# Kernel tuning notes

Measured on AMD Instinct MI355X. Metric: run time of the kernel, lower is better.

The kernel has to match this reference:

```python
import jax, jax.numpy as jnp
import numpy as np

N = 100000   # nodes
E = 3200000  # edges
F = 128      # input features
H1 = 128     # first_gcn_dimensions
H2 = 64      # second_gcn_dimensions
D1 = 64      # first_dense_neurons
D2 = 8       # second_dense_neurons
L = 10       # number_of_labels


def setup_inputs() -> dict:
    key = jax.random.key(0)
    ks = jax.random.split(key, 8)
    edges = jax.random.randint(ks[0], (2, E), 0, N)
    features = jax.random.normal(ks[1], (N, F), dtype=jnp.float32)
    s = lambda k, shape: jax.random.normal(k, shape, dtype=jnp.float32) * 0.05
    return dict(
        edges=edges, features=features,
        W1=s(ks[2], (F, H1)), b1=jnp.zeros((H1,), jnp.float32),
        W2=s(ks[3], (H1, H2)), b2=jnp.zeros((H2,), jnp.float32),
        Wf1=s(ks[4], (H2, D1)), bf1=jnp.zeros((D1,), jnp.float32),
        Wf2=s(ks[5], (D1, D2)), bf2=jnp.zeros((D2,), jnp.float32),
        Wl=s(ks[6], (H2 * D2, L)), bl=jnp.zeros((L,), jnp.float32),
    )


def gcn_conv(x, W, b, src, dst, n):
    # PyG GCNConv: x' = D^{-1/2} (A + I) D^{-1/2} (x W) + b  (self-loops already in src/dst)
    h = x @ W                                            # [N, out]
    deg = jax.ops.segment_sum(jnp.ones(dst.shape[0], x.dtype), dst, num_segments=n)
    dinv = jnp.where(deg > 0, jax.lax.rsqrt(deg), 0.0)   # deg^{-1/2}, 0 for isolated
    norm = dinv[src] * dinv[dst]                         # [E+N]
    agg = jax.ops.segment_sum(h[src] * norm[:, None], dst, num_segments=n)
    return agg + b


def reference(edges, features, W1, b1, W2, b2, Wf1, bf1, Wf2, bf2, Wl, bl):
    n = features.shape[0]
    loop = jnp.arange(n)
    src = jnp.concatenate([edges[0], loop])
    dst = jnp.concatenate([edges[1], loop])

    h1 = jax.nn.relu(gcn_conv(features, W1, b1, src, dst, n))  # [N, H1]
    h2 = gcn_conv(h1, W2, b2, src, dst, n)                     # [N, H2]

    a1 = jnp.tanh(h2 @ Wf1 + bf1)                              # [N, D1]
    att = jax.nn.softmax(a1 @ Wf2 + bf2, axis=0)               # softmax over nodes, [N, D2]

    graph_embedding = (att.T @ h2).reshape(1, -1)              # [1, D2*H2]
    P = att.T @ att - jnp.eye(att.shape[1], dtype=att.dtype)   # [D2, D2]
    penalty = jnp.sum(jnp.sqrt(jnp.sum(P * P, axis=1)))

    predictions = jax.nn.log_softmax(graph_embedding @ Wl + bl, axis=1)  # [1, L]
    return graph_embedding, penalty, predictions
```

## Files before the change

### kernel.cpp

```cpp
#include <hip/hip_runtime.h>
#include <hip/hip_bf16.h>
#include <math.h>

#define NNODES 100000
#define NEDGES 3200000
#define NBUK ((NNODES + 127) >> 7)
#define NCHUNK 256
#define EPC (NEDGES / NCHUNK)

typedef float floatx2 __attribute__((ext_vector_type(2)));
typedef float f32x4 __attribute__((ext_vector_type(4)));
typedef short bf16x8 __attribute__((ext_vector_type(8)));

__device__ __forceinline__ unsigned short f2bf(float x) {
    unsigned u = __float_as_uint(x);
    unsigned r = u + 0x7FFFu + ((u >> 16) & 1u);
    return (unsigned short)(r >> 16);
}

__device__ __forceinline__ void acc8_fp8(uint2 v, floatx2* a) {
    a[0] += __builtin_amdgcn_cvt_pk_f32_fp8(v.x, false);
    a[1] += __builtin_amdgcn_cvt_pk_f32_fp8(v.x, true);
    a[2] += __builtin_amdgcn_cvt_pk_f32_fp8(v.y, false);
    a[3] += __builtin_amdgcn_cvt_pk_f32_fp8(v.y, true);
}
__device__ __forceinline__ void acc4_fp8(unsigned v, floatx2* a) {
    a[0] += __builtin_amdgcn_cvt_pk_f32_fp8(v, false);
    a[1] += __builtin_amdgcn_cvt_pk_f32_fp8(v, true);
}

__global__ void prep_w_kernel(const float* __restrict__ W1, const float* __restrict__ W2,
                              unsigned short* __restrict__ Wt1, unsigned short* __restrict__ Wt2) {
    int i = blockIdx.x * 256 + threadIdx.x;
    if (i < 128 * 128) {
        int k = i >> 7, n = i & 127;
        Wt1[n * 128 + k] = f2bf(W1[i]);
    } else if (i < 128 * 128 + 128 * 64) {
        int j = i - 128 * 128;
        int k = j >> 6, n = j & 63;
        Wt2[n * 128 + k] = f2bf(W2[j]);
    }
}

__global__ __launch_bounds__(1024) void chunk_hist_kernel(const int* __restrict__ dst,
                                                          int* __restrict__ hist) {
    __shared__ int h[NBUK];
    int c = blockIdx.x, t = threadIdx.x;
    for (int i = t; i < NBUK; i += 1024) h[i] = 0;
    __syncthreads();
    const int4* d4 = (const int4*)(dst + c * EPC);
    for (int i = t; i < EPC / 4; i += 1024) {
        int4 d = d4[i];
        atomicAdd(&h[d.x >> 7], 1);
        atomicAdd(&h[d.y >> 7], 1);
        atomicAdd(&h[d.z >> 7], 1);
        atomicAdd(&h[d.w >> 7], 1);
    }
    __syncthreads();
    for (int i = t; i < NBUK; i += 1024)
        hist[c * NBUK + i] = h[i];
}

__global__ void col_scan_kernel(int* __restrict__ hist, int* __restrict__ btot) {
    int t = blockIdx.x * 256 + threadIdx.x;
    if (t >= NBUK) return;
    int run = 0;
    for (int c = 0; c < NCHUNK; c++) {
        int idx = c * NBUK + t;
        int v = hist[idx];
        hist[idx] = run;
        run += v;
    }
    btot[t] = run;
}

__global__ void bucket_scan_kernel(const int* __restrict__ btot, int* __restrict__ bstart,
                                   int* __restrict__ row_start, float* __restrict__ smalls) {
    __shared__ int s[1024];
    int t = threadIdx.x;
    if (t < 592) smalls[t] = 0.0f;
    int v = (t < NBUK) ? btot[t] : 0;
    s[t] = v;
    __syncthreads();
    for (int off = 1; off < 1024; off <<= 1) {
        int x = (t >= off) ? s[t - off] : 0;
        __syncthreads();
        s[t] += x;
        __syncthreads();
    }
    if (t < NBUK) bstart[t] = s[t] - v;
    if (t == 0) {
        bstart[NBUK] = NEDGES;
        row_start[NNODES] = NEDGES;
    }
}

__global__ __launch_bounds__(1024) void chunk_scatter_kernel(const int* __restrict__ src,
                                                             const int* __restrict__ dst,
                                                             const int* __restrict__ hist,
                                                             const int* __restrict__ bstart,
                                                             int* __restrict__ ebuk) {
    __shared__ int cur[NBUK];
    int c = blockIdx.x, t = threadIdx.x;
    for (int i = t; i < NBUK; i += 1024)
        cur[i] = bstart[i] + hist[c * NBUK + i];
    __syncthreads();
    const int4* s4 = (const int4*)(src + c * EPC);
    const int4* d4 = (const int4*)(dst + c * EPC);
    for (int i = t; i < EPC / 4; i += 1024) {
        int4 s = s4[i];
        int4 d = d4[i];
        int p0 = atomicAdd(&cur[d.x >> 7], 1);
        ebuk[p0] = s.x | ((d.x & 127) << 20);
        int p1 = atomicAdd(&cur[d.y >> 7], 1);
        ebuk[p1] = s.y | ((d.y & 127) << 20);
        int p2 = atomicAdd(&cur[d.z >> 7], 1);
        ebuk[p2] = s.z | ((d.z & 127) << 20);
        int p3 = atomicAdd(&cur[d.w >> 7], 1);
        ebuk[p3] = s.w | ((d.w & 127) << 20);
    }
}

__global__ __launch_bounds__(256) void build_kernel(const int* __restrict__ ebuk,
                                                    const int* __restrict__ bstart,
                                                    int* __restrict__ row_start,
                                                    float* __restrict__ dinv,
                                                    int* __restrict__ csr) {
    __shared__ int cnt[128];
    __shared__ int scn[128];
    __shared__ int cur[128];
    int b = blockIdx.x;
    int t = threadIdx.x;
    int s0 = bstart[b], s1 = bstart[b + 1];
    if (t < 128) cnt[t] = 0;
    __syncthreads();
    for (int i = s0 + t; i < s1; i += 256)
        atomicAdd(&cnt[(ebuk[i] >> 20) & 127], 1);
    __syncthreads();
    if (t < 128) scn[t] = cnt[t];
    __syncthreads();
#pragma unroll
    for (int off = 1; off < 128; off <<= 1) {
        int x = (t < 128 && t >= off) ? scn[t - off] : 0;
        __syncthreads();
        if (t < 128) scn[t] += x;
        __syncthreads();
    }
    int node = b * 128 + t;
    if (t < 128) {
        int rs = s0 + scn[t] - cnt[t];
        cur[t] = rs;
        if (node < NNODES) {
            row_start[node] = rs;
            dinv[node] = rsqrtf((float)cnt[t] + 1.0f);
        }
    }
    __syncthreads();
    for (int i = s0 + t; i < s1; i += 256) {
        int v = ebuk[i];
        int pos = atomicAdd(&cur[(v >> 20) & 127], 1);
        csr[pos] = v & 0xFFFFF;
    }
}

template <int KIN, int KOUT, bool ABF16>
__global__ __launch_bounds__(256) void gemm_mfma_kernel(const void* __restrict__ Av,
                                                        const unsigned short* __restrict__ Wt,
                                                        const float* __restrict__ rowscale,
                                                        unsigned char* __restrict__ stage) {
    constexpr int LDK = KIN + 8;
    constexpr int LDC = KOUT + 4;
    constexpr int SH_AB = (64 + KOUT) * LDK * 2;
    constexpr int SH_C  = 64 * LDC * 4;
    constexpr int SH = SH_AB > SH_C ? SH_AB : SH_C;
    __shared__ char shbuf[SH];
    unsigned short* As = (unsigned short*)shbuf;
    unsigned short* Ws = As + 64 * LDK;
    float* Cs = (float*)shbuf;
    int t = threadIdx.x;
    int block_row = blockIdx.x * 64;

    for (int idx = t; idx < KOUT * (KIN / 8); idx += 256) {
        int n = idx / (KIN / 8), c = idx % (KIN / 8);
        *(uint4*)(Ws + n * LDK + c * 8) = *(const uint4*)(Wt + n * KIN + c * 8);
    }
    if (ABF16) {
        const unsigned short* A = (const unsigned short*)Av;
        for (int idx = t; idx < 64 * (KIN / 8); idx += 256) {
            int r = idx / (KIN / 8), c = idx % (KIN / 8);
            uint4 v = make_uint4(0, 0, 0, 0);
            if (block_row + r < NNODES)
                v = *(const uint4*)(A + (size_t)(block_row + r) * KIN + c * 8);
            *(uint4*)(As + r * LDK + c * 8) = v;
        }
    } else {
        const float* A = (const float*)Av;
        for (int idx = t; idx < 64 * (KIN / 4); idx += 256) {
            int r = idx / (KIN / 4), c = idx % (KIN / 4);
            float4 v = make_float4(0.f, 0.f, 0.f, 0.f);
            if (block_row + r < NNODES)
                v = *(const float4*)(A + (size_t)(block_row + r) * KIN + c * 4);
            unsigned p0 = (unsigned)f2bf(v.x) | ((unsigned)f2bf(v.y) << 16);
            unsigned p1 = (unsigned)f2bf(v.z) | ((unsigned)f2bf(v.w) << 16);
            *(uint2*)(As + r * LDK + c * 4) = make_uint2(p0, p1);
        }
    }
    __syncthreads();

    int wv = t >> 6, lane = t & 63;
    int r0 = wv * 16;
    int m = lane & 15, q = lane >> 4;
    constexpr int NT = KOUT / 16;
    constexpr int KS = KIN / 32;
    f32x4 acc[NT];
#pragma unroll
    for (int nt = 0; nt < NT; nt++) acc[nt] = (f32x4)(0.f);
    bf16x8 afr[KS];
#pragma unroll
    for (int ks = 0; ks < KS; ks++)
        afr[ks] = *(bf16x8*)(As + (r0 + m) * LDK + ks * 32 + q * 8);
#pragma unroll
    for (int nt = 0; nt < NT; nt++) {
#pragma unroll
        for (int ks = 0; ks < KS; ks++) {
            bf16x8 b = *(bf16x8*)(Ws + (nt * 16 + m) * LDK + ks * 32 + q * 8);
            acc[nt] = __builtin_amdgcn_mfma_f32_16x16x32_bf16(afr[ks], b, acc[nt], 0, 0, 0);
        }
    }
    __syncthreads();
#pragma unroll
    for (int nt = 0; nt < NT; nt++)
#pragma unroll
        for (int j = 0; j < 4; j++)
            Cs[(r0 + q * 4 + j) * LDC + nt * 16 + m] = acc[nt][j];
    __syncthreads();
    for (int idx = t; idx < 64 * (KOUT / 4); idx += 256) {
        int r = idx / (KOUT / 4), c4 = idx % (KOUT / 4);
        int row = block_row + r;
        if (row < NNODES) {
            float4 v = *(float4*)(Cs + r * LDC + c4 * 4);
            float d = rowscale[row];
            int pk = __builtin_amdgcn_cvt_pk_fp8_f32(v.x * d, v.y * d, 0, false);
            pk = __builtin_amdgcn_cvt_pk_fp8_f32(v.z * d, v.w * d, pk, true);
            *(unsigned*)(stage + (size_t)row * KOUT + c4 * 4) = (unsigned)pk;
        }
    }
}

__global__ __launch_bounds__(256) void gather128_kernel(
    const unsigned char* __restrict__ hs, const int* __restrict__ row_start,
    const int* __restrict__ csr, const float* __restrict__ dinv,
    const float* __restrict__ bias, unsigned short* __restrict__ out) {
    int wave = threadIdx.x >> 6;
    int lane = threadIdx.x & 63;
    int n = blockIdx.x * 4 + wave;
    if (n >= NNODES) return;
    int g = lane >> 4;
    int c = lane & 15;
    unsigned boff = (unsigned)c << 3;
    int start = row_start[n], end = row_start[n + 1];
    floatx2 acc[4];
#pragma unroll
    for (int i = 0; i < 4; i++) acc[i] = (floatx2)(0.f);
    int w = (start + 3) & ~3;
    if (w > end) w = end;
    {
        int e2 = start + g;
        if (e2 < w) {
            unsigned o = ((unsigned)csr[e2] << 7) + boff;
            acc8_fp8(*(const uint2*)(hs + o), acc);
        }
    }
    for (; w + 32 <= end; w += 32) {
        int4 ca = *(const int4*)(csr + w + 4 * g);
        int4 cbv = *(const int4*)(csr + w + 16 + 4 * g);
        uint2 v0 = *(const uint2*)(hs + (((unsigned)ca.x  << 7) + boff));
        uint2 v1 = *(const uint2*)(hs + (((unsigned)ca.y  << 7) + boff));
        uint2 v2 = *(const uint2*)(hs + (((unsigned)ca.z  << 7) + boff));
        uint2 v3 = *(const uint2*)(hs + (((unsigned)ca.w  << 7) + boff));
        uint2 v4 = *(const uint2*)(hs + (((unsigned)cbv.x << 7) + boff));
        uint2 v5 = *(const uint2*)(hs + (((unsigned)cbv.y << 7) + boff));
        uint2 v6 = *(const uint2*)(hs + (((unsigned)cbv.z << 7) + boff));
        uint2 v7 = *(const uint2*)(hs + (((unsigned)cbv.w << 7) + boff));
        acc8_fp8(v0, acc); acc8_fp8(v1, acc); acc8_fp8(v2, acc); acc8_fp8(v3, acc);
        acc8_fp8(v4, acc); acc8_fp8(v5, acc); acc8_fp8(v6, acc); acc8_fp8(v7, acc);
    }
    for (; w + 16 <= end; w += 16) {
        int4 cs = *(const int4*)(csr + w + 4 * g);
        uint2 v0 = *(const uint2*)(hs + (((unsigned)cs.x << 7) + boff));
        uint2 v1 = *(const uint2*)(hs + (((unsigned)cs.y << 7) + boff));
        uint2 v2 = *(const uint2*)(hs + (((unsigned)cs.z << 7) + boff));
        uint2 v3 = *(const uint2*)(hs + (((unsigned)cs.w << 7) + boff));
        acc8_fp8(v0, acc); acc8_fp8(v1, acc); acc8_fp8(v2, acc); acc8_fp8(v3, acc);
    }
    for (int e2 = w + g; e2 < end; e2 += 4) {
        unsigned o = ((unsigned)csr[e2] << 7) + boff;
        acc8_fp8(*(const uint2*)(hs + o), acc);
    }
#pragma unroll
    for (int off = 16; off <= 32; off <<= 1)
#pragma unroll
        for (int i = 0; i < 4; i++) {
            acc[i].x += __shfl_xor(acc[i].x, off);
            acc[i].y += __shfl_xor(acc[i].y, off);
        }
    if (g == 0) {
        floatx2 s[4];
#pragma unroll
        for (int i = 0; i < 4; i++) s[i] = (floatx2)(0.f);
        acc8_fp8(*(const uint2*)(hs + (((unsigned)n << 7) + boff)), s);
        float d = dinv[n];
        int j = c * 8;
        float4 b0 = *(const float4*)(bias + j);
        float4 b1 = *(const float4*)(bias + j + 4);
        float r0 = fmaxf((acc[0].x + s[0].x) * d + b0.x, 0.f);
        float r1 = fmaxf((acc[0].y + s[0].y) * d + b0.y, 0.f);
        float r2 = fmaxf((acc[1].x + s[1].x) * d + b0.z, 0.f);
        float r3 = fmaxf((acc[1].y + s[1].y) * d + b0.w, 0.f);
        float r4 = fmaxf((acc[2].x + s[2].x) * d + b1.x, 0.f);
        float r5 = fmaxf((acc[2].y + s[2].y) * d + b1.y, 0.f);
        float r6 = fmaxf((acc[3].x + s[3].x) * d + b1.z, 0.f);
        float r7 = fmaxf((acc[3].y + s[3].y) * d + b1.w, 0.f);
        uint4 p;
        p.x = (unsigned)f2bf(r0) | ((unsigned)f2bf(r1) << 16);
        p.y = (unsigned)f2bf(r2) | ((unsigned)f2bf(r3) << 16);
        p.z = (unsigned)f2bf(r4) | ((unsigned)f2bf(r5) << 16);
        p.w = (unsigned)f2bf(r6) | ((unsigned)f2bf(r7) << 16);
        *(uint4*)(out + (((size_t)n << 7) + j)) = p;
    }
}

__global__ __launch_bounds__(256) void gather64_kernel(
    const unsigned char* __restrict__ hs, const int* __restrict__ row_start,
    const int* __restrict__ csr, const float* __restrict__ dinv,
    const float* __restrict__ bias, float* __restrict__ out) {
    int wave = threadIdx.x >> 6;
    int lane = threadIdx.x & 63;
    int n = blockIdx.x * 4 + wave;
    if (n >= NNODES) return;
    int g = lane >> 4;
    int c = lane & 15;
    unsigned boff = (unsigned)c << 2;
    int start = row_start[n], end = row_start[n + 1];
    floatx2 acc[2];
    acc[0] = (floatx2)(0.f); acc[1] = (floatx2)(0.f);
    int w = (start + 3) & ~3;
    if (w > end) w = end;
    {
        int e2 = start + g;
        if (e2 < w) {
            unsigned o = ((unsigned)csr[e2] << 6) + boff;
            acc4_fp8(*(const unsigned*)(hs + o), acc);
        }
    }
    for (; w + 32 <= end; w += 32) {
        int4 ca = *(const int4*)(csr + w + 4 * g);
        int4 cbv = *(const int4*)(csr + w + 16 + 4 * g);
        unsigned v0 = *(const unsigned*)(hs + (((unsigned)ca.x  << 6) + boff));
        unsigned v1 = *(const unsigned*)(hs + (((unsigned)ca.y  << 6) + boff));
        unsigned v2 = *(const unsigned*)(hs + (((unsigned)ca.z  << 6) + boff));
        unsigned v3 = *(const unsigned*)(hs + (((unsigned)ca.w  << 6) + boff));
        unsigned v4 = *(const unsigned*)(hs + (((unsigned)cbv.x << 6) + boff));
        unsigned v5 = *(const unsigned*)(hs + (((unsigned)cbv.y << 6) + boff));
        unsigned v6 = *(const unsigned*)(hs + (((unsigned)cbv.z << 6) + boff));
        unsigned v7 = *(const unsigned*)(hs + (((unsigned)cbv.w << 6) + boff));
        acc4_fp8(v0, acc); acc4_fp8(v1, acc); acc4_fp8(v2, acc); acc4_fp8(v3, acc);
        acc4_fp8(v4, acc); acc4_fp8(v5, acc); acc4_fp8(v6, acc); acc4_fp8(v7, acc);
    }
    for (; w + 16 <= end; w += 16) {
        int4 cs = *(const int4*)(csr + w + 4 * g);
        unsigned v0 = *(const unsigned*)(hs + (((unsigned)cs.x << 6) + boff));
        unsigned v1 = *(const unsigned*)(hs + (((unsigned)cs.y << 6) + boff));
        unsigned v2 = *(const unsigned*)(hs + (((unsigned)cs.z << 6) + boff));
        unsigned v3 = *(const unsigned*)(hs + (((unsigned)cs.w << 6) + boff));
        acc4_fp8(v0, acc); acc4_fp8(v1, acc); acc4_fp8(v2, acc); acc4_fp8(v3, acc);
    }
    for (int e2 = w + g; e2 < end; e2 += 4) {
        unsigned o = ((unsigned)csr[e2] << 6) + boff;
        acc4_fp8(*(const unsigned*)(hs + o), acc);
    }
#pragma unroll
    for (int off = 16; off <= 32; off <<= 1)
#pragma unroll
        for (int i = 0; i < 2; i++) {
            acc[i].x += __shfl_xor(acc[i].x, off);
            acc[i].y += __shfl_xor(acc[i].y, off);
        }
    if (g == 0) {
        floatx2 s[2];
        s[0] = (floatx2)(0.f); s[1] = (floatx2)(0.f);
        acc4_fp8(*(const unsigned*)(hs + (((unsigned)n << 6) + boff)), s);
        float d = dinv[n];
        int j = c * 4;
        float4 b4 = *(const float4*)(bias + j);
        float4 r;
        r.x = (acc[0].x + s[0].x) * d + b4.x;
        r.y = (acc[0].y + s[0].y) * d + b4.y;
        r.z = (acc[1].x + s[1].x) * d + b4.z;
        r.w = (acc[1].y + s[1].y) * d + b4.w;
        *(float4*)(out + (((size_t)n << 6) + j)) = r;
    }
}

__global__ __launch_bounds__(256) void attnpool_kernel(const float* __restrict__ h2,
                                                       const float* __restrict__ Wf1,
                                                       const float* __restrict__ bf1,
                                                       const float* __restrict__ Wf2,
                                                       const float* __restrict__ bf2,
                                                       float* __restrict__ ge,
                                                       float* __restrict__ ata,
                                                       float* __restrict__ colsum) {
    __shared__ float h2S[64][68];
    __shared__ float a1S[64][68];
    __shared__ float attS[64][8];
    __shared__ float colS[8][64];
    int t = threadIdx.x;
    int d0 = t >> 6;
    int j  = t & 63;
    int de = t >> 3, ee = t & 7;
    float accge0 = 0.f, accge1 = 0.f, accata = 0.f, acccol = 0.f;
    int ntiles = (NNODES + 63) / 64;
    for (int tile = blockIdx.x; tile < ntiles; tile += gridDim.x) {
        int base = tile * 64;
#pragma unroll
        for (int q = 0; q < 4; q++) {
            int idx = t + q * 256;
            int r = idx >> 4, cc = (idx & 15) * 4;
            int row = base + r;
            float4 v = (row < NNODES) ? *(const float4*)(h2 + (size_t)row * 64 + cc)
                                      : make_float4(0.f, 0.f, 0.f, 0.f);
            *(float4*)(&h2S[r][cc]) = v;
        }
        __syncthreads();
        {
            int cg = t & 15, rg = t >> 4;
            int jj = cg * 4, r0 = rg * 4;
            float4 b4 = *(const float4*)(bf1 + jj);
            float4 acc[4];
#pragma unroll
            for (int r = 0; r < 4; r++) acc[r] = b4;
#pragma unroll 4
            for (int k = 0; k < 64; k++) {
                float4 wv = *(const float4*)(Wf1 + (size_t)k * 64 + jj);
#pragma unroll
                for (int r = 0; r < 4; r++) {
                    float a = h2S[r0 + r][k];
                    acc[r].x += a * wv.x; acc[r].y += a * wv.y;
                    acc[r].z += a * wv.z; acc[r].w += a * wv.w;
                }
            }
#pragma unroll
            for (int r = 0; r < 4; r++) {
                a1S[r0 + r][jj]     = tanhf(acc[r].x);
                a1S[r0 + r][jj + 1] = tanhf(acc[r].y);
                a1S[r0 + r][jj + 2] = tanhf(acc[r].z);
                a1S[r0 + r][jj + 3] = tanhf(acc[r].w);
            }
        }
        __syncthreads();
        {
            int cc = t & 7, r = t >> 3;
#pragma unroll
            for (int h = 0; h < 2; h++) {
                int rr = r + h * 32;
                float acc = bf2[cc];
                for (int k = 0; k < 64; k++)
                    acc += a1S[rr][k] * Wf2[(size_t)k * 8 + cc];
                float ev = (base + rr < NNODES) ? __expf(acc) : 0.f;
                attS[rr][cc] = ev;
                colS[cc][rr] = ev;
            }
        }
        __syncthreads();
#pragma unroll 8
        for (int i = 0; i < 64; i++) {
            float hv = h2S[i][j];
            accge0 += attS[i][d0] * hv;
            accge1 += attS[i][d0 + 4] * hv;
        }
        if (t < 64) {
#pragma unroll 8
            for (int i = 0; i < 64; i++) accata += attS[i][de] * attS[i][ee];
        }
        if (t < 8) {
            float s = 0.f;
#pragma unroll
            for (int r = 0; r < 64; r++) s += colS[t][r];
            acccol += s;
        }
        __syncthreads();
    }
    atomicAdd(ge + d0 * 64 + j, accge0);
    atomicAdd(ge + (d0 + 4) * 64 + j, accge1);
    if (t < 64) atomicAdd(ata + de * 8 + ee, accata);
    if (t < 8) atomicAdd(colsum + t, acccol);
}

__global__ void final_kernel(const float* __restrict__ geacc, const float* __restrict__ ata,
                             const float* __restrict__ colsum, const float* __restrict__ Wl,
                             const float* __restrict__ bl, float* __restrict__ out) {
    __shared__ float geF[512];
    __shared__ float inv[8];
    __shared__ float logits[10];
    int t = threadIdx.x;
    if (t < 8) inv[t] = 1.0f / colsum[t];
    __syncthreads();
    for (int idx = t; idx < 512; idx += 64) {
        int d = idx >> 6;
        float v = geacc[idx] * inv[d];
        geF[idx] = v;
        out[idx] = v;
    }
    __syncthreads();
    if (t == 0) {
        float pen = 0.f;
        for (int d = 0; d < 8; d++) {
            float s = 0.f;
            for (int e = 0; e < 8; e++) {
                float p = ata[d * 8 + e] * inv[d] * inv[e] - (d == e ? 1.0f : 0.0f);
                s += p * p;
            }
            pen += sqrtf(s);
        }
        out[512] = pen;
    }
    if (t < 10) {
        float acc = bl[t];
        for (int k = 0; k < 512; k++) acc += geF[k] * Wl[(size_t)k * 10 + t];
        logits[t] = acc;
    }
    __syncthreads();
    if (t == 0) {
        float m = -INFINITY;
        for (int l = 0; l < 10; l++) m = fmaxf(m, logits[l]);
        float s = 0.f;
        for (int l = 0; l < 10; l++) s += expf(logits[l] - m);
        float ls = logf(s);
        for (int l = 0; l < 10; l++) out[513 + l] = logits[l] - m - ls;
    }
}

extern "C" void kernel_launch(void* const* d_in, const int* in_sizes, int n_in,
                              void* d_out, int out_size, void* d_ws, size_t ws_size,
                              hipStream_t stream) {
    const int* esrc = (const int*)d_in[0];
    const int* edst = esrc + NEDGES;
    const float* X   = (const float*)d_in[1];
    const float* W1  = (const float*)d_in[2];
    const float* b1  = (const float*)d_in[3];
    const float* W2  = (const float*)d_in[4];
    const float* b2  = (const float*)d_in[5];
    const float* Wf1 = (const float*)d_in[6];
    const float* bf1 = (const float*)d_in[7];
    const float* Wf2 = (const float*)d_in[8];
    const float* bf2 = (const float*)d_in[9];
    const float* Wl  = (const float*)d_in[10];
    const float* bl  = (const float*)d_in[11];
    float* out = (float*)d_out;

    float* ws     = (float*)d_ws;
    float* dinv   = ws;
    float* smalls = ws + 100352;
    float* colsum = smalls + 8;
    float* ata    = smalls + 16;
    float* geacc  = smalls + 80;
    float* A = ws + 101376;
    float* B = A + (size_t)NNODES * 128;
    int* row_start = (int*)(B + (size_t)NNODES * 128);
    int* btot      = row_start + 100352;
    int* bstart    = btot + 1024;
    int* csr       = bstart + 1024;
    unsigned short* Wt1 = (unsigned short*)(csr + NEDGES);
    unsigned short* Wt2 = Wt1 + 128 * 128;
    int* ebuk      = (int*)A;
    int* hist      = (int*)B;
    unsigned char* stage = (unsigned char*)A;
    unsigned short* h1 = (unsigned short*)B;
    float* h2  = B;

    prep_w_kernel<<<96, 256, 0, stream>>>(W1, W2, Wt1, Wt2);

    chunk_hist_kernel<<<NCHUNK, 1024, 0, stream>>>(edst, hist);
    col_scan_kernel<<<4, 256, 0, stream>>>(hist, btot);
    bucket_scan_kernel<<<1, 1024, 0, stream>>>(btot, bstart, row_start, smalls);
    chunk_scatter_kernel<<<NCHUNK, 1024, 0, stream>>>(esrc, edst, hist, bstart, ebuk);
    build_kernel<<<NBUK, 256, 0, stream>>>(ebuk, bstart, row_start, dinv, csr);

    gemm_mfma_kernel<128, 128, false><<<(NNODES + 63) / 64, 256, 0, stream>>>(X, Wt1, dinv, stage);
    gather128_kernel<<<(NNODES + 3) / 4, 256, 0, stream>>>(stage, row_start, csr, dinv, b1, h1);

    gemm_mfma_kernel<128, 64, true><<<(NNODES + 63) / 64, 256, 0, stream>>>(h1, Wt2, dinv, stage);
    gather64_kernel<<<(NNODES + 3) / 4, 256, 0, stream>>>(stage, row_start, csr, dinv, b2, h2);

    attnpool_kernel<<<512, 256, 0, stream>>>(h2, Wf1, bf1, Wf2, bf2, geacc, ata, colsum);
    final_kernel<<<1, 64, 0, stream>>>(geacc, ata, colsum, Wl, bl, out);
}
```

Baseline: 424.5 us.

## Parallelize column scan per bucket and widen gather unrolling and per-lane loads

The column scan over chunk histograms becomes one block per bucket doing a shared-memory scan across chunks, replacing the serial per-thread loop that ran on only 4 blocks. gather128 doubles its main-loop unroll to 64 edges per iteration. gather64 now gives each lane 8 bytes (8 lanes per row, 8 edge groups) instead of 4 bytes, and also unrolls to 64 edges. These aim to expose more memory-level parallelism in the edge gathers and remove the latency-bound serial scan, at the cost of more registers and more tail work on low-degree nodes.

```diff
diff --git a/kernel.cpp b/kernel.cpp
--- a/kernel.cpp
+++ b/kernel.cpp
@@ -23,10 +23,6 @@
     a[1] += __builtin_amdgcn_cvt_pk_f32_fp8(v.x, true);
     a[2] += __builtin_amdgcn_cvt_pk_f32_fp8(v.y, false);
     a[3] += __builtin_amdgcn_cvt_pk_f32_fp8(v.y, true);
-}
-__device__ __forceinline__ void acc4_fp8(unsigned v, floatx2* a) {
-    a[0] += __builtin_amdgcn_cvt_pk_f32_fp8(v, false);
-    a[1] += __builtin_amdgcn_cvt_pk_f32_fp8(v, true);
 }
 
 __global__ void prep_w_kernel(const float* __restrict__ W1, const float* __restrict__ W2,
@@ -61,17 +57,23 @@
         hist[c * NBUK + i] = h[i];
 }
 
-__global__ void col_scan_kernel(int* __restrict__ hist, int* __restrict__ btot) {
-    int t = blockIdx.x * 256 + threadIdx.x;
-    if (t >= NBUK) return;
-    int run = 0;
-    for (int c = 0; c < NCHUNK; c++) {
-        int idx = c * NBUK + t;
-        int v = hist[idx];
-        hist[idx] = run;
-        run += v;
-    }
-    btot[t] = run;
+__global__ __launch_bounds__(256) void col_scan_kernel(int* __restrict__ hist,
+                                                       int* __restrict__ btot) {
+    __shared__ int sdat[NCHUNK];
+    int b = blockIdx.x;
+    int t = threadIdx.x;
+    int v = hist[t * NBUK + b];
+    sdat[t] = v;
+    __syncthreads();
+#pragma unroll
+    for (int off = 1; off < NCHUNK; off <<= 1) {
+        int x = (t >= off) ? sdat[t - off] : 0;
+        __syncthreads();
+        sdat[t] += x;
+        __syncthreads();
+    }
+    hist[t * NBUK + b] = sdat[t] - v;
+    if (t == NCHUNK - 1) btot[b] = sdat[t];
 }
 
 __global__ void bucket_scan_kernel(const int* __restrict__ btot, int* __restrict__ bstart,
@@ -271,19 +273,32 @@
             acc8_fp8(*(const uint2*)(hs + o), acc);
         }
     }
-    for (; w + 32 <= end; w += 32) {
-        int4 ca = *(const int4*)(csr + w + 4 * g);
-        int4 cbv = *(const int4*)(csr + w + 16 + 4 * g);
-        uint2 v0 = *(const uint2*)(hs + (((unsigned)ca.x  << 7) + boff));
-        uint2 v1 = *(const uint2*)(hs + (((unsigned)ca.y  << 7) + boff));
-        uint2 v2 = *(const uint2*)(hs + (((unsigned)ca.z  << 7) + boff));
-        uint2 v3 = *(const uint2*)(hs + (((unsigned)ca.w  << 7) + boff));
-        uint2 v4 = *(const uint2*)(hs + (((unsigned)cbv.x << 7) + boff));
-        uint2 v5 = *(const uint2*)(hs + (((unsigned)cbv.y << 7) + boff));
-        uint2 v6 = *(const uint2*)(hs + (((unsigned)cbv.z << 7) + boff));
-        uint2 v7 = *(const uint2*)(hs + (((unsigned)cbv.w << 7) + boff));
-        acc8_fp8(v0, acc); acc8_fp8(v1, acc); acc8_fp8(v2, acc); acc8_fp8(v3, acc);
-        acc8_fp8(v4, acc); acc8_fp8(v5, acc); acc8_fp8(v6, acc); acc8_fp8(v7, acc);
+    for (; w + 64 <= end; w += 64) {
+        const int* cp = csr + w + 16 * g;
+        int4 ca = *(const int4*)(cp);
+        int4 cb = *(const int4*)(cp + 4);
+        int4 cc = *(const int4*)(cp + 8);
+        int4 cd = *(const int4*)(cp + 12);
+        uint2 v0  = *(const uint2*)(hs + (((unsigned)ca.x << 7) + boff));
+        uint2 v1  = *(const uint2*)(hs + (((unsigned)ca.y << 7) + boff));
+        uint2 v2  = *(const uint2*)(hs + (((unsigned)ca.z << 7) + boff));
+        uint2 v3  = *(const uint2*)(hs + (((unsigned)ca.w << 7) + boff));
+        uint2 v4  = *(const uint2*)(hs + (((unsigned)cb.x << 7) + boff));
+        uint2 v5  = *(const uint2*)(hs + (((unsigned)cb.y << 7) + boff));
+        uint2 v6  = *(const uint2*)(hs + (((unsigned)cb.z << 7) + boff));
+        uint2 v7  = *(const uint2*)(hs + (((unsigned)cb.w << 7) + boff));
+        uint2 v8  = *(const uint2*)(hs + (((unsigned)cc.x << 7) + boff));
+        uint2 v9  = *(const uint2*)(hs + (((unsigned)cc.y << 7) + boff));
+        uint2 v10 = *(const uint2*)(hs + (((unsigned)cc.z << 7) + boff));
+        uint2 v11 = *(const uint2*)(hs + (((unsigned)cc.w << 7) + boff));
+        uint2 v12 = *(const uint2*)(hs + (((unsigned)cd.x << 7) + boff));
+        uint2 v13 = *(const uint2*)(hs + (((unsigned)cd.y << 7) + boff));
+        uint2 v14 = *(const uint2*)(hs + (((unsigned)cd.z << 7) + boff));
+        uint2 v15 = *(const uint2*)(hs + (((unsigned)cd.w << 7) + boff));
+        acc8_fp8(v0, acc);  acc8_fp8(v1, acc);  acc8_fp8(v2, acc);  acc8_fp8(v3, acc);
+        acc8_fp8(v4, acc);  acc8_fp8(v5, acc);  acc8_fp8(v6, acc);  acc8_fp8(v7, acc);
+        acc8_fp8(v8, acc);  acc8_fp8(v9, acc);  acc8_fp8(v10, acc); acc8_fp8(v11, acc);
+        acc8_fp8(v12, acc); acc8_fp8(v13, acc); acc8_fp8(v14, acc); acc8_fp8(v15, acc);
     }
     for (; w + 16 <= end; w += 16) {
         int4 cs = *(const int4*)(csr + w + 4 * g);
@@ -338,67 +353,75 @@
     int lane = threadIdx.x & 63;
     int n = blockIdx.x * 4 + wave;
     if (n >= NNODES) return;
-    int g = lane >> 4;
-    int c = lane & 15;
-    unsigned boff = (unsigned)c << 2;
+    int g = lane >> 3;
+    int c = lane & 7;
+    unsigned boff = (unsigned)c << 3;
     int start = row_start[n], end = row_start[n + 1];
-    floatx2 acc[2];
-    acc[0] = (floatx2)(0.f); acc[1] = (floatx2)(0.f);
+    floatx2 acc[4];
+#pragma unroll
+    for (int i = 0; i < 4; i++) acc[i] = (floatx2)(0.f);
     int w = (start + 3) & ~3;
     if (w > end) w = end;
     {
         int e2 = start + g;
         if (e2 < w) {
             unsigned o = ((unsigned)csr[e2] << 6) + boff;
-            acc4_fp8(*(const unsigned*)(hs + o), acc);
-        }
-    }
-    for (; w + 32 <= end; w += 32) {
-        int4 ca = *(const int4*)(csr + w + 4 * g);
-        int4 cbv = *(const int4*)(csr + w + 16 + 4 * g);
-        unsigned v0 = *(const unsigned*)(hs + (((unsigned)ca.x  << 6) + boff));
-        unsigned v1 = *(const unsigned*)(hs + (((unsigned)ca.y  << 6) + boff));
-        unsigned v2 = *(const unsigned*)(hs + (((unsigned)ca.z  << 6) + boff));
-        unsigned v3 = *(const unsigned*)(hs + (((unsigned)ca.w  << 6) + boff));
-        unsigned v4 = *(const unsigned*)(hs + (((unsigned)cbv.x << 6) + boff));
-        unsigned v5 = *(const unsigned*)(hs + (((unsigned)cbv.y << 6) + boff));
-        unsigned v6 = *(const unsigned*)(hs + (((unsigned)cbv.z << 6) + boff));
-        unsigned v7 = *(const unsigned*)(hs + (((unsigned)cbv.w << 6) + boff));
-        acc4_fp8(v0, acc); acc4_fp8(v1, acc); acc4_fp8(v2, acc); acc4_fp8(v3, acc);
-        acc4_fp8(v4, acc); acc4_fp8(v5, acc); acc4_fp8(v6, acc); acc4_fp8(v7, acc);
+            acc8_fp8(*(const uint2*)(hs + o), acc);
+        }
+    }
+    for (; w + 64 <= end; w += 64) {
+        const int* cp = csr + w + 8 * g;
+        int4 ca = *(const int4*)(cp);
+        int4 cb = *(const int4*)(cp + 4);
+        uint2 v0 = *(const uint2*)(hs + (((unsigned)ca.x << 6) + boff));
+        uint2 v1 = *(const uint2*)(hs + (((unsigned)ca.y << 6) + boff));
+        uint2 v2 = *(const uint2*)(hs + (((unsigned)ca.z << 6) + boff));
+        uint2 v3 = *(const uint2*)(hs + (((unsigned)ca.w << 6) + boff));
+        uint2 v4 = *(const uint2*)(hs + (((unsigned)cb.x << 6) + boff));
+        uint2 v5 = *(const uint2*)(hs + (((unsigned)cb.y << 6) + boff));
+        uint2 v6 = *(const uint2*)(hs + (((unsigned)cb.z << 6) + boff));
+        uint2 v7 = *(const uint2*)(hs + (((unsigned)cb.w << 6) + boff));
+        acc8_fp8(v0, acc); acc8_fp8(v1, acc); acc8_fp8(v2, acc); acc8_fp8(v3, acc);
+        acc8_fp8(v4, acc); acc8_fp8(v5, acc); acc8_fp8(v6, acc); acc8_fp8(v7, acc);
     }
     for (; w + 16 <= end; w += 16) {
-        int4 cs = *(const int4*)(csr + w + 4 * g);
-        unsigned v0 = *(const unsigned*)(hs + (((unsigned)cs.x << 6) + boff));
-        unsigned v1 = *(const unsigned*)(hs + (((unsigned)cs.y << 6) + boff));
-        unsigned v2 = *(const unsigned*)(hs + (((unsigned)cs.z << 6) + boff));
-        unsigned v3 = *(const unsigned*)(hs + (((unsigned)cs.w << 6) + boff));
-        acc4_fp8(v0, acc); acc4_fp8(v1, acc); acc4_fp8(v2, acc); acc4_fp8(v3, acc);
-    }
-    for (int e2 = w + g; e2 < end; e2 += 4) {
+        int2 cs = *(const int2*)(csr + w + 2 * g);
+        uint2 v0 = *(const uint2*)(hs + (((unsigned)cs.x << 6) + boff));
+        uint2 v1 = *(const uint2*)(hs + (((unsigned)cs.y << 6) + boff));
+        acc8_fp8(v0, acc); acc8_fp8(v1, acc);
+    }
+    for (int e2 = w + g; e2 < end; e2 += 8) {
         unsigned o = ((unsigned)csr[e2] << 6) + boff;
-        acc4_fp8(*(const unsigned*)(hs + o), acc);
-    }
-#pragma unroll
-    for (int off = 16; off <= 32; off <<= 1)
-#pragma unroll
-        for (int i = 0; i < 2; i++) {
+        acc8_fp8(*(const uint2*)(hs + o), acc);
+    }
+#pragma unroll
+    for (int off = 8; off <= 32; off <<= 1)
+#pragma unroll
+        for (int i = 0; i < 4; i++) {
             acc[i].x += __shfl_xor(acc[i].x, off);
             acc[i].y += __shfl_xor(acc[i].y, off);
         }
     if (g == 0) {
-        floatx2 s[2];
-        s[0] = (floatx2)(0.f); s[1] = (floatx2)(0.f);
-        acc4_fp8(*(const unsigned*)(hs + (((unsigned)n << 6) + boff)), s);
+        floatx2 s[4];
+#pragma unroll
+        for (int i = 0; i < 4; i++) s[i] = (floatx2)(0.f);
+        acc8_fp8(*(const uint2*)(hs + (((unsigned)n << 6) + boff)), s);
         float d = dinv[n];
-        int j = c * 4;
-        float4 b4 = *(const float4*)(bias + j);
-        float4 r;
-        r.x = (acc[0].x + s[0].x) * d + b4.x;
-        r.y = (acc[0].y + s[0].y) * d + b4.y;
-        r.z = (acc[1].x + s[1].x) * d + b4.z;
-        r.w = (acc[1].y + s[1].y) * d + b4.w;
-        *(float4*)(out + (((size_t)n << 6) + j)) = r;
+        int j = c * 8;
+        float4 b0 = *(const float4*)(bias + j);
+        float4 b1 = *(const float4*)(bias + j + 4);
+        float4 o0, o1;
+        o0.x = (acc[0].x + s[0].x) * d + b0.x;
+        o0.y = (acc[0].y + s[0].y) * d + b0.y;
+        o0.z = (acc[1].x + s[1].x) * d + b0.z;
+        o0.w = (acc[1].y + s[1].y) * d + b0.w;
+        o1.x = (acc[2].x + s[2].x) * d + b1.x;
+        o1.y = (acc[2].y + s[2].y) * d + b1.y;
+        o1.z = (acc[3].x + s[3].x) * d + b1.z;
+        o1.w = (acc[3].y + s[3].y) * d + b1.w;
+        float* op = out + (((size_t)n << 6) + j);
+        *(float4*)op = o0;
+        *(float4*)(op + 4) = o1;
     }
 }
 
@@ -581,7 +604,7 @@
     prep_w_kernel<<<96, 256, 0, stream>>>(W1, W2, Wt1, Wt2);
 
     chunk_hist_kernel<<<NCHUNK, 1024, 0, stream>>>(edst, hist);
-    col_scan_kernel<<<4, 256, 0, stream>>>(hist, btot);
+    col_scan_kernel<<<NBUK, 256, 0, stream>>>(hist, btot);
     bucket_scan_kernel<<<1, 1024, 0, stream>>>(btot, bstart, row_start, smalls);
     chunk_scatter_kernel<<<NCHUNK, 1024, 0, stream>>>(esrc, edst, hist, bstart, ebuk);
     build_kernel<<<NBUK, 256, 0, stream>>>(ebuk, bstart, row_start, dinv, csr);
```

Measured after the change: 421.4 us. Within noise of the previous version (-0.8%).
